# Kernel optimization log

Hardware: AMD Instinct MI355X
Metric: run time of the kernel (lower is better)

The kernel has to match this reference:

```python
import jax, jax.numpy as jnp
import numpy as np
from jax import lax

MAX_DISP = 4  # patch_size = 2*MAX_DISP+1 = 9; kernel_size=1, stride=1, padding=0


def setup_inputs() -> dict:
    key = jax.random.key(0)
    k1, k2 = jax.random.split(key)
    B, C, H, W = 4, 256, 96, 96
    feat1 = jax.random.normal(k1, (B, C, H, W), dtype=jnp.float32)
    feat2 = jax.random.normal(k2, (B, C, H, W), dtype=jnp.float32)
    return {"feat1": feat1, "feat2": feat2}


def _cost_volume(feat1, feat2):
    # SpatialCorrelationSampler with kernel_size=1, patch_size=2*MAX_DISP+1,
    # stride=1, padding=0: for each displacement (dy,dx) in [-d,d]^2,
    # corr[b,dy,dx,y,x] = sum_c feat1[b,c,y,x] * feat2[b,c,y+dy,x+dx]
    # (out-of-bounds feat2 treated as zero). Output reshaped to [B, P*P, H, W].
    B, C, H, W = feat1.shape
    d = MAX_DISP
    P = 2 * d + 1
    f2_pad = jnp.pad(feat2, ((0, 0), (0, 0), (d, d), (d, d)))
    # flattened displacement offsets into the padded map, shape [P*P, 2]
    dy, dx = jnp.meshgrid(jnp.arange(P), jnp.arange(P), indexing="ij")
    offsets = jnp.stack([dy.ravel(), dx.ravel()], axis=-1)  # [P*P, 2]

    def step(carry, off):
        f2 = lax.dynamic_slice(f2_pad, (0, 0, off[0], off[1]), (B, C, H, W))
        corr = jnp.einsum("bchw,bchw->bhw", feat1, f2)  # sum over channels
        return carry, corr

    _, cv = lax.scan(step, None, offsets)  # [P*P, B, H, W]
    return jnp.transpose(cv, (1, 0, 2, 3))  # [B, P*P, H, W]


def reference(feat1, feat2):
    return _cost_volume(feat1, feat2)
```

## Files before the change

kernel.cpp:

```cpp
#include <hip/hip_runtime.h>


typedef _Float16 f16x8 __attribute__((ext_vector_type(8)));
typedef float f32x4 __attribute__((ext_vector_type(4)));

#define NB 4
#define NC 256
#define NH 96
#define NW 96
#define NP 9
#define PLANE (NH * NW)
#define TENS (NB * NH * NW * NC)
#define WS_NEED ((unsigned long long)TENS * 2ull)
#define TPT4 (TENS / 32)
#define PACK_BLK (TPT4 / 256)
#define MAIN_BLK 2304
#define CGSTR (NW * 8)
#define ROWSTR (32 * CGSTR)
#define AROW 272
#define LPAD 37

__global__ __launch_bounds__(256) void pack_f2(const float* __restrict__ f2,
                                               _Float16* __restrict__ ws)
{
    const int e   = blockIdx.x * 256 + threadIdx.x;
    const int row = e / 768;
    const int q   = e % 768;
    const int cg  = q / 24;
    const int x4  = q % 24;
    const int b   = row / NH;
    const int y   = row % NH;

    const float* sp = f2 + ((size_t)(b * NC + cg * 8) * NH + y) * NW + x4 * 4;
    float vv[8][4];
#pragma unroll
    for (int j = 0; j < 8; ++j) {
        const float4 v = *(const float4*)(sp + (size_t)j * PLANE);
        vv[j][0] = v.x; vv[j][1] = v.y; vv[j][2] = v.z; vv[j][3] = v.w;
    }
    _Float16* dp = ws + ((size_t)row * 32 + cg) * CGSTR + (size_t)x4 * 32;
#pragma unroll
    for (int xi = 0; xi < 4; ++xi) {
        f16x8 o;
#pragma unroll
        for (int j = 0; j < 8; ++j) o[j] = (_Float16)vv[j][xi];
        *(f16x8*)(dp + xi * 8) = o;
    }
}

__global__ __launch_bounds__(384) void costvol_mfma(const float* __restrict__ f1,
                                                    const _Float16* __restrict__ f2p,
                                                    float* __restrict__ out)
{
    __shared__ _Float16 lds_a[16 * AROW];
    __shared__ float ldso[81][20];

    const int bid = blockIdx.x;
    const int swz = (bid & 7) * (MAIN_BLK / 8) + (bid >> 3);
    const int mt  = swz % 6;
    const int y   = (swz / 6) % 96;
    const int b   = swz / 576;

    const int w    = threadIdx.x >> 6;
    const int lane = threadIdx.x & 63;
    const int lr   = lane & 15;
    const int lg   = lane >> 4;
    const int m0   = mt * 16;
    const int d3   = w >> 1;
    const int tl   = w & 1;

#pragma unroll
    for (int i = 0; i < 3; ++i) {
        const int task = threadIdx.x + i * 384;
        if (task < 1024) {
            const int c  = task >> 2;
            const int xq = task & 3;
            const float4 v = *(const float4*)(
                f1 + ((size_t)(b * NC + c) * NH + y) * NW + m0 + xq * 4);
            _Float16* d0 = lds_a + (size_t)(xq * 4) * AROW + c;
            d0[0 * AROW] = (_Float16)v.x;
            d0[1 * AROW] = (_Float16)v.y;
            d0[2 * AROW] = (_Float16)v.z;
            d0[3 * AROW] = (_Float16)v.w;
        }
    }
    __syncthreads();

    f16x8 a[8];
    {
        const _Float16* ap = lds_a + (size_t)lr * AROW + lg * 8;
#pragma unroll
        for (int ks = 0; ks < 8; ++ks) a[ks] = *(const f16x8*)(ap + ks * 32);
    }

    const int n0   = m0 + (tl ? 8 : -8) + lr;
    const bool inN = tl ? (n0 < 96) : (n0 >= 0);
    const int dxoف = 0;
    const f16x8 bz = {};

#pragma unroll 1
    for (int i = 0; i < 3; ++i) {
        const int dy = d3 * 3 + i;
        const int y2 = y + dy - 4;
        f32x4 acc = {0.f, 0.f, 0.f, 0.f};

        if (y2 >= 0 && y2 < 96) {
            const _Float16* pb = f2p + (size_t)(b * 96 + y2) * ROWSTR
                               + (size_t)lg * CGSTR + (ptrdiff_t)n0 * 8;
            f16x8 B[8];
#pragma unroll
            for (int ks = 0; ks < 8; ++ks)
                B[ks] = inN ? *(const f16x8*)(pb + (size_t)ks * 4 * CGSTR) : bz;
#pragma unroll
            for (int ks = 0; ks < 8; ++ks)
                acc = __builtin_amdgcn_mfma_f32_16x16x32_f16(a[ks], B[ks], acc, 0, 0, 0);
        }

#pragma unroll
        for (int reg = 0; reg < 4; ++reg) {
            const int mrow = lg * 4 + reg;
            const int dx   = lr - mrow + (tl ? 12 : -4);
            if (dx >= 0 && dx <= 8) ldso[dy * 9 + dx][mrow] = acc[reg];
        }
    }

    __syncthreads();

    const int r = threadIdx.x >> 2;
    const int q = (threadIdx.x & 3) * 4;
    if (r < 81) {
        const float4 v = make_float4(ldso[r][q], ldso[r][q + 1],
                                     ldso[r][q + 2], ldso[r][q + 3]);
        *(float4*)(out + ((size_t)(b * 81 + r) * PLANE) + y * 96 + m0 + q) = v;
    }
}

__global__ __launch_bounds__(256) void costvol_f32(const float* __restrict__ f1,
                                                   const float* __restrict__ f2,
                                                   float* __restrict__ out)
{
    __shared__ float lds[2 * 64 * LPAD];
    const int bid = blockIdx.x;
    const int swz = (bid & 7) * (1296 / 8) + (bid >> 3);
    const int dyi = swz % NP;
    const int g   = swz / NP;
    const int w    = threadIdx.x >> 6;
    const int lane = threadIdx.x & 63;
    const int chk = g * 64 + lane;
    const int b   = chk / (NH * 24);
    const int rem = chk - b * (NH * 24);
    const int y   = rem / 24;
    const int x0  = (rem - y * 24) * 4;
    const int y2  = y + dyi - 4;

    float acc[NP][4];
#pragma unroll
    for (int i = 0; i < NP; ++i)
#pragma unroll
        for (int j = 0; j < 4; ++j) acc[i][j] = 0.f;

    if (y2 >= 0 && y2 < NH) {
        const float* p1 = f1 + ((size_t)(b * NC + w * 64) * NH + y) * NW + x0;
        const float* p2 = f2 + ((size_t)(b * NC + w * 64) * NH + y2) * NW + x0;
        const bool hasL = (x0 >= 4);
        const bool hasR = (x0 <= NW - 8);
#pragma unroll 4
        for (int c = 0; c < 64; ++c) {
            const float4 av = *(const float4*)p1;
            const float4 Lv = hasL ? *(const float4*)(p2 - 4) : make_float4(0.f, 0.f, 0.f, 0.f);
            const float4 Mv = *(const float4*)(p2);
            const float4 Rv = hasR ? *(const float4*)(p2 + 4) : make_float4(0.f, 0.f, 0.f, 0.f);
            const float wv[12] = {Lv.x, Lv.y, Lv.z, Lv.w, Mv.x, Mv.y, Mv.z, Mv.w,
                                  Rv.x, Rv.y, Rv.z, Rv.w};
            const float aa[4] = {av.x, av.y, av.z, av.w};
#pragma unroll
            for (int dxi = 0; dxi < NP; ++dxi)
#pragma unroll
                for (int j = 0; j < 4; ++j) acc[dxi][j] += aa[j] * wv[dxi + j];
            p1 += PLANE;
            p2 += PLANE;
        }
    }

    float* reg0 = &lds[0 * 64 * LPAD + lane * LPAD];
    float* reg1 = &lds[1 * 64 * LPAD + lane * LPAD];
    if (w >= 2) {
        float* dst = (w == 2) ? reg0 : reg1;
#pragma unroll
        for (int dxi = 0; dxi < NP; ++dxi)
#pragma unroll
            for (int j = 0; j < 4; ++j) dst[dxi * 4 + j] = acc[dxi][j];
    }
    __syncthreads();
    if (w < 2) {
        const float* src = (w == 0) ? reg0 : reg1;
#pragma unroll
        for (int dxi = 0; dxi < NP; ++dxi)
#pragma unroll
            for (int j = 0; j < 4; ++j) acc[dxi][j] += src[dxi * 4 + j];
    }
    __syncthreads();
    if (w == 1) {
#pragma unroll
        for (int dxi = 0; dxi < NP; ++dxi)
#pragma unroll
            for (int j = 0; j < 4; ++j) reg0[dxi * 4 + j] = acc[dxi][j];
    }
    __syncthreads();
    if (w == 0) {
#pragma unroll
        for (int dxi = 0; dxi < NP; ++dxi)
#pragma unroll
            for (int j = 0; j < 4; ++j) acc[dxi][j] += reg0[dxi * 4 + j];
        float* ob = out + ((size_t)(b * 81 + dyi * 9) * NH + y) * NW + x0;
#pragma unroll
        for (int dxi = 0; dxi < NP; ++dxi) {
            *(float4*)ob = make_float4(acc[dxi][0], acc[dxi][1], acc[dxi][2], acc[dxi][3]);
            ob += PLANE;
        }
    }
}

extern "C" void kernel_launch(void* const* d_in, const int* in_sizes, int n_in,
                              void* d_out, int out_size, void* d_ws, size_t ws_size,
                              hipStream_t stream) {
    const float* f1 = (const float*)d_in[0];
    const float* f2 = (const float*)d_in[1];
    float* out = (float*)d_out;
    if (ws_size >= WS_NEED) {
        _Float16* ws = (_Float16*)d_ws;
        pack_f2<<<dim3(PACK_BLK, 1, 1), dim3(256, 1, 1), 0, stream>>>(f2, ws);
        costvol_mfma<<<dim3(MAIN_BLK, 1, 1), dim3(384, 1, 1), 0, stream>>>(f1, ws, out);
    } else {
        costvol_f32<<<dim3(1296, 1, 1), dim3(256, 1, 1), 0, stream>>>(f1, f2, out);
    }
}
```

Measured before the change: 38.95 us.

## Process two output rows per block to reuse loaded feat2 rows across both

```diff
diff --git a/kernel.cpp b/kernel.cpp
--- a/kernel.cpp
+++ b/kernel.cpp
@@ -14,7 +14,7 @@
 #define WS_NEED ((unsigned long long)TENS * 2ull)
 #define TPT4 (TENS / 32)
 #define PACK_BLK (TPT4 / 256)
-#define MAIN_BLK 2304
+#define MAIN_BLK 1152
 #define CGSTR (NW * 8)
 #define ROWSTR (32 * CGSTR)
 #define AROW 272
@@ -48,36 +48,37 @@
     }
 }
 
-__global__ __launch_bounds__(384) void costvol_mfma(const float* __restrict__ f1,
+__global__ __launch_bounds__(320) void costvol_mfma(const float* __restrict__ f1,
                                                     const _Float16* __restrict__ f2p,
                                                     float* __restrict__ out)
 {
-    __shared__ _Float16 lds_a[16 * AROW];
-    __shared__ float ldso[81][20];
+    __shared__ _Float16 lds_a[2][16 * AROW];
+    __shared__ float ldso[2][81][20];
 
     const int bid = blockIdx.x;
     const int swz = (bid & 7) * (MAIN_BLK / 8) + (bid >> 3);
     const int mt  = swz % 6;
-    const int y   = (swz / 6) % 96;
-    const int b   = swz / 576;
+    const int yp  = (swz / 6) % 48;
+    const int b   = swz / 288;
+    const int y0  = yp * 2;
 
     const int w    = threadIdx.x >> 6;
     const int lane = threadIdx.x & 63;
     const int lr   = lane & 15;
     const int lg   = lane >> 4;
     const int m0   = mt * 16;
-    const int d3   = w >> 1;
-    const int tl   = w & 1;
-
-#pragma unroll
-    for (int i = 0; i < 3; ++i) {
-        const int task = threadIdx.x + i * 384;
-        if (task < 1024) {
-            const int c  = task >> 2;
-            const int xq = task & 3;
+
+#pragma unroll
+    for (int i = 0; i < 7; ++i) {
+        const int t = threadIdx.x + i * 320;
+        if (t < 2048) {
+            const int yloc = t >> 10;
+            const int r    = t & 1023;
+            const int c    = r >> 2;
+            const int xq   = r & 3;
             const float4 v = *(const float4*)(
-                f1 + ((size_t)(b * NC + c) * NH + y) * NW + m0 + xq * 4);
-            _Float16* d0 = lds_a + (size_t)(xq * 4) * AROW + c;
+                f1 + ((size_t)(b * NC + c) * NH + (y0 + yloc)) * NW + m0 + xq * 4);
+            _Float16* d0 = lds_a[yloc] + (size_t)(xq * 4) * AROW + c;
             d0[0 * AROW] = (_Float16)v.x;
             d0[1 * AROW] = (_Float16)v.y;
             d0[2 * AROW] = (_Float16)v.z;
@@ -86,52 +87,73 @@
     }
     __syncthreads();
 
-    f16x8 a[8];
-    {
-        const _Float16* ap = lds_a + (size_t)lr * AROW + lg * 8;
-#pragma unroll
-        for (int ks = 0; ks < 8; ++ks) a[ks] = *(const f16x8*)(ap + ks * 32);
-    }
-
-    const int n0   = m0 + (tl ? 8 : -8) + lr;
-    const bool inN = tl ? (n0 < 96) : (n0 >= 0);
-    const int dxoف = 0;
+    f16x8 a[2][8];
+#pragma unroll
+    for (int yloc = 0; yloc < 2; ++yloc) {
+        const _Float16* ap = lds_a[yloc] + (size_t)lr * AROW + lg * 8;
+#pragma unroll
+        for (int ks = 0; ks < 8; ++ks) a[yloc][ks] = *(const f16x8*)(ap + ks * 32);
+    }
+
     const f16x8 bz = {};
-
-#pragma unroll 1
-    for (int i = 0; i < 3; ++i) {
-        const int dy = d3 * 3 + i;
-        const int y2 = y + dy - 4;
-        f32x4 acc = {0.f, 0.f, 0.f, 0.f};
-
-        if (y2 >= 0 && y2 < 96) {
-            const _Float16* pb = f2p + (size_t)(b * 96 + y2) * ROWSTR
-                               + (size_t)lg * CGSTR + (ptrdiff_t)n0 * 8;
-            f16x8 B[8];
-#pragma unroll
-            for (int ks = 0; ks < 8; ++ks)
-                B[ks] = inN ? *(const f16x8*)(pb + (size_t)ks * 4 * CGSTR) : bz;
-#pragma unroll
-            for (int ks = 0; ks < 8; ++ks)
-                acc = __builtin_amdgcn_mfma_f32_16x16x32_f16(a[ks], B[ks], acc, 0, 0, 0);
-        }
-
-#pragma unroll
-        for (int reg = 0; reg < 4; ++reg) {
-            const int mrow = lg * 4 + reg;
-            const int dx   = lr - mrow + (tl ? 12 : -4);
-            if (dx >= 0 && dx <= 8) ldso[dy * 9 + dx][mrow] = acc[reg];
-        }
-    }
-
-    __syncthreads();
-
-    const int r = threadIdx.x >> 2;
+    const int y2a = y0 - 4 + 2 * w;
+
+#pragma unroll
+    for (int rr = 0; rr < 2; ++rr) {
+        const int y2  = y2a + rr;
+        const int dys = 2 * w + rr;
+        const bool val0 = (dys <= 8);
+        const bool val1 = (dys >= 1);
+        const bool inb  = (y2 >= 0) && (y2 < 96);
+        const _Float16* rbase = f2p + (size_t)(b * 96 + (inb ? y2 : 0)) * ROWSTR
+                              + (size_t)lg * CGSTR;
+#pragma unroll
+        for (int tl = 0; tl < 2; ++tl) {
+            const int n0   = m0 + (tl ? 8 : -8) + lr;
+            const bool inN = tl ? (n0 < 96) : (n0 >= 0);
+            f32x4 acc0 = {0.f, 0.f, 0.f, 0.f};
+            f32x4 acc1 = {0.f, 0.f, 0.f, 0.f};
+
+            if (inb) {
+                const _Float16* pb = rbase + (ptrdiff_t)n0 * 8;
+                f16x8 B[8];
+#pragma unroll
+                for (int ks = 0; ks < 8; ++ks)
+                    B[ks] = inN ? *(const f16x8*)(pb + (size_t)ks * 4 * CGSTR) : bz;
+                if (val0) {
+#pragma unroll
+                    for (int ks = 0; ks < 8; ++ks)
+                        acc0 = __builtin_amdgcn_mfma_f32_16x16x32_f16(a[0][ks], B[ks], acc0, 0, 0, 0);
+                }
+                if (val1) {
+#pragma unroll
+                    for (int ks = 0; ks < 8; ++ks)
+                        acc1 = __builtin_amdgcn_mfma_f32_16x16x32_f16(a[1][ks], B[ks], acc1, 0, 0, 0);
+                }
+            }
+
+#pragma unroll
+            for (int reg = 0; reg < 4; ++reg) {
+                const int mrow = lg * 4 + reg;
+                const int dx   = lr - mrow + (tl ? 12 : -4);
+                if (dx >= 0 && dx <= 8) {
+                    if (val0) ldso[0][dys * 9 + dx][mrow] = acc0[reg];
+                    if (val1) ldso[1][(dys - 1) * 9 + dx][mrow] = acc1[reg];
+                }
+            }
+        }
+    }
+
+    __syncthreads();
+
     const int q = (threadIdx.x & 3) * 4;
-    if (r < 81) {
-        const float4 v = make_float4(ldso[r][q], ldso[r][q + 1],
-                                     ldso[r][q + 2], ldso[r][q + 3]);
-        *(float4*)(out + ((size_t)(b * 81 + r) * PLANE) + y * 96 + m0 + q) = v;
+#pragma unroll
+    for (int ri = threadIdx.x >> 2; ri < 162; ri += 80) {
+        const int yloc = ri / 81;
+        const int r    = ri - yloc * 81;
+        const float4 v = make_float4(ldso[yloc][r][q], ldso[yloc][r][q + 1],
+                                     ldso[yloc][r][q + 2], ldso[yloc][r][q + 3]);
+        *(float4*)(out + ((size_t)(b * 81 + r) * PLANE) + (y0 + yloc) * 96 + m0 + q) = v;
     }
 }
 
@@ -230,7 +252,7 @@
     if (ws_size >= WS_NEED) {
         _Float16* ws = (_Float16*)d_ws;
         pack_f2<<<dim3(PACK_BLK, 1, 1), dim3(256, 1, 1), 0, stream>>>(f2, ws);
-        costvol_mfma<<<dim3(MAIN_BLK, 1, 1), dim3(384, 1, 1), 0, stream>>>(f1, ws, out);
+        costvol_mfma<<<dim3(MAIN_BLK, 1, 1), dim3(320, 1, 1), 0, stream>>>(f1, ws, out);
     } else {
         costvol_f32<<<dim3(1296, 1, 1), dim3(256, 1, 1), 0, stream>>>(f1, f2, out);
     }
```

Result: no change. 39.38 us (+1.1%).
